# Optimization experiments

Measured on AMD Instinct MI355X. Metric: run time of the kernel, lower is better.

The kernel has to match this reference:

```python
import jax, jax.numpy as jnp
import numpy as np

B, CIN, COUT = 8, 8, 8
NX, NT = 512, 512
M1, M2 = 4, 4


def setup_inputs() -> dict:
    key = jax.random.key(0)
    k1, k2, k3 = jax.random.split(key, 3)
    scale = 1.0 / (CIN * COUT)
    x = jax.random.normal(k1, (B, CIN, NX, NT), dtype=jnp.float32)
    T = jnp.arange(NT, dtype=jnp.float32).reshape(1, NT)  # time grid
    X = jnp.arange(NX, dtype=jnp.float32).reshape(1, NX)  # space grid
    weights1_ri = scale * jax.random.uniform(k2, (CIN, COUT, M1, M2, 2), dtype=jnp.float32)
    weights2_ri = scale * jax.random.uniform(k3, (CIN, COUT, M1, M2, 2), dtype=jnp.float32)
    return {"x": x, "T": T, "X": X, "weights1_ri": weights1_ri, "weights2_ri": weights2_ri}


def reference(x, T, X, weights1_ri, weights2_ri):
    # subsample every other grid point (as in the torch forward)
    xs = x[:, :, ::2, ::2]                      # [B, Cin, Hs, Ws]
    tx = T[:, ::2]                              # [1, Ws]
    ty = X[:, ::2]                              # [1, Hs]
    dty = ty[0, 1] - ty[0, 0]
    dtx = tx[0, 1] - tx[0, 0]
    Hs, Ws = xs.shape[-2], xs.shape[-1]
    Wr = Ws // 2 + 1

    FW1 = jnp.fft.rfft2(xs)                     # [B, Cin, Hs, Wr] complex64

    two_pi_i = 2.0 * jnp.pi * 1j
    lam1 = (jnp.fft.fftfreq(Hs).astype(jnp.float32) / dty).astype(jnp.complex64) * two_pi_i   # [Hs]
    lam2 = (jnp.fft.rfftfreq(Ws).astype(jnp.float32) / dtx).astype(jnp.complex64) * two_pi_i  # [Wr]

    w1 = (weights1_ri[..., 0] + 1j * weights1_ri[..., 1]).astype(jnp.complex64)
    w2 = (weights2_ri[..., 0] + 1j * weights2_ri[..., 1]).astype(jnp.complex64)

    out2 = jnp.zeros((xs.shape[0], w1.shape[1], Hs, Wr), dtype=jnp.complex64)
    out2 = out2.at[:, :, :M1, :M2].set(
        jnp.einsum('bixy,ioxy->boxy', FW1[:, :, :M1, :M2], w1))
    out2 = out2.at[:, :, -M1:, :M2].set(
        jnp.einsum('bixy,ioxy->boxy', FW1[:, :, -M1:, :M2], w2))

    # inverse transform onto the FULL (non-subsampled) grid via complex exponentials.
    # Same math as the original rank-4 term6 einsum, factorized separably.
    E1 = jnp.exp(lam1[:, None] * X.astype(jnp.complex64).reshape(1, -1))  # [Hs, NX]
    E2 = jnp.exp(lam2[:, None] * T.astype(jnp.complex64).reshape(1, -1))  # [Wr, NT]

    tmp = jnp.einsum('boxw,xz->bozw', out2, E1)   # [B, Cout, NX, Wr]
    x2 = jnp.einsum('bozw,wi->bozi', tmp, E2)     # [B, Cout, NX, NT]
    return jnp.real(x2) / (Ws * Hs)
```

## Files before the change

### kernel.cpp

```cpp
#include <hip/hip_runtime.h>
#include <hip/hip_bf16.h>


#define PI2 6.283185307179586f

typedef float vfloat4 __attribute__((ext_vector_type(4)));

__device__ __forceinline__ float foldred(float u, float v, int msk, int lane) {
    float send = (lane & msk) ? u : v;
    float recv = __shfl_xor(send, msk, 64);
    return ((lane & msk) ? v : u) + recv;
}

__device__ __forceinline__ float fold8(const float* ar, const float* ai, int lane) {
    float A0 = foldred(ar[0], ai[0], 1, lane);
    float A1 = foldred(ar[1], ai[1], 1, lane);
    float A2 = foldred(ar[2], ai[2], 1, lane);
    float A3 = foldred(ar[3], ai[3], 1, lane);
    float B0 = foldred(A0, A1, 2, lane);
    float B1 = foldred(A2, A3, 2, lane);
    float C  = foldred(B0, B1, 4, lane);
    C += __shfl_xor(C, 8, 64);
    C += __shfl_xor(C, 16, 64);
    C += __shfl_xor(C, 32, 64);
    return C;
}

__global__ __launch_bounds__(256, 8) void k_fused(const float* __restrict__ x,
                                                  const float* __restrict__ w1,
                                                  const float* __restrict__ w2,
                                                  float* __restrict__ Yg,
                                                  unsigned int* __restrict__ done,
                                                  float* __restrict__ out) {
    __shared__ float vals[4][64];
    __shared__ float lcf[64];

    int lane = threadIdx.x & 63;
    int w    = threadIdx.x >> 6;
    int b    = blockIdx.x & 7;
    int t    = blockIdx.x >> 3;

    {
        int ci = t >> 5, g = t & 31;
        int bc = b * 8 + ci;
        int y0 = g * 8 + w * 2;

        const vfloat4* r0 = (const vfloat4*)(x + ((size_t)bc * 512 + (size_t)(2 * y0)) * 512);
        const vfloat4* r1 = (const vfloat4*)(x + ((size_t)bc * 512 + (size_t)(2 * y0 + 2)) * 512);
        vfloat4 a0 = __builtin_nontemporal_load(&r0[lane]);
        vfloat4 a1 = __builtin_nontemporal_load(&r0[lane + 64]);
        vfloat4 b0 = __builtin_nontemporal_load(&r1[lane]);
        vfloat4 b1 = __builtin_nontemporal_load(&r1[lane + 64]);

        float s, c;
        sincosf((PI2 / 128.0f) * (float)lane, &s, &c);
        float er[4], ei[4], orE[4], oiE[4];
        er[0] = 1.f; ei[0] = 0.f;
        er[1] = c;   ei[1] = -s;
        er[2] = er[1]*er[1] - ei[1]*ei[1];  ei[2] = 2.f*er[1]*ei[1];
        er[3] = er[2]*er[1] - ei[2]*ei[1];  ei[3] = er[2]*ei[1] + ei[2]*er[1];
        const float rr1 = 0.999698818696204f, ri1 = -0.024541228522912f;
        const float rr2 = 0.998795456205172f, ri2 = -0.049067674327418f;
        const float rr3 = 0.997290456678690f, ri3 = -0.073564563599667f;
        orE[0] = 1.f; oiE[0] = 0.f;
        orE[1] = er[1]*rr1 - ei[1]*ri1;  oiE[1] = er[1]*ri1 + ei[1]*rr1;
        orE[2] = er[2]*rr2 - ei[2]*ri2;  oiE[2] = er[2]*ri2 + ei[2]*rr2;
        orE[3] = er[3]*rr3 - ei[3]*ri3;  oiE[3] = er[3]*ri3 + ei[3]*rr3;

        float arA[4], aiA[4], arB[4], aiB[4];
#pragma unroll
        for (int kw = 0; kw < 4; ++kw) {
            float sgn = (kw & 1) ? -1.f : 1.f;
            float eA = a0[0] + sgn * a1[0], oA = a0[2] + sgn * a1[2];
            float eB = b0[0] + sgn * b1[0], oB = b0[2] + sgn * b1[2];
            arA[kw] = eA * er[kw] + oA * orE[kw];
            aiA[kw] = eA * ei[kw] + oA * oiE[kw];
            arB[kw] = eB * er[kw] + oB * orE[kw];
            aiB[kw] = eB * ei[kw] + oB * oiE[kw];
        }
        float Ca = fold8(arA, aiA, lane);
        float Cb = fold8(arB, aiB, lane);

        int midx = lane >> 3;
        float mf = (midx < 4) ? (float)midx : (float)(midx - 8);
        float snm, csm;
        sincosf((PI2 / 256.0f) * mf * (float)y0, &snm, &csm);
        float ty0 = -snm;
        float smm, cmm;
        sincosf((PI2 / 256.0f) * mf, &smm, &cmm);
        float cs1 = csm * cmm + ty0 * smm;
        float ty1 = ty0 * cmm - csm * smm;

        float pa = __shfl_xor(Ca, 1, 64);
        float pb = __shfl_xor(Cb, 1, 64);
        float selA = (lane & 1) ? ty0 : -ty0;
        float selB = (lane & 1) ? ty1 : -ty1;
        vals[w][lane] = Ca * csm + pa * selA + Cb * cs1 + pb * selB;
        __syncthreads();

        if (threadIdx.x < 64) {
            float sum = vals[0][lane] + vals[1][lane] + vals[2][lane] + vals[3][lane];
            __hip_atomic_store(&Yg[((size_t)((b * 32 + g) * 8 + ci)) * 64 + lane], sum,
                               __ATOMIC_RELEASE, __HIP_MEMORY_SCOPE_AGENT);
        }
        __syncthreads();
        if (threadIdx.x == 0)
            __hip_atomic_fetch_add(&done[b], 1u, __ATOMIC_RELEASE, __HIP_MEMORY_SCOPE_AGENT);
    }

    if (threadIdx.x == 0) {
        while (__hip_atomic_load(&done[b], __ATOMIC_ACQUIRE, __HIP_MEMORY_SCOPE_AGENT) < 256u)
            __builtin_amdgcn_s_sleep(2);
    }
    __syncthreads();

    int o     = t >> 5;
    int chunk = t & 31;
    int bo    = b * 8 + o;

    {
        int midx = lane >> 3, kw = (lane >> 1) & 3, ri = lane & 1, mx = midx & 3;
        const float* wt = (midx < 4) ? w1 : w2;
        float wr_[8], swi_[8];
#pragma unroll
        for (int ci = 0; ci < 8; ++ci) {
            const float* wp = wt + ((((ci * 8 + o) * 4 + mx) * 4 + kw) * 2);
            wr_[ci]  = wp[0];
            swi_[ci] = ri ? wp[1] : -wp[1];
        }
        float acc = 0.f;
#pragma unroll
        for (int gi = 0; gi < 8; ++gi) {
            int g = w + gi * 4;
            float* Yp = Yg + ((size_t)((b * 32 + g) * 8)) * 64 + lane;
#pragma unroll
            for (int ci = 0; ci < 8; ++ci) {
                float Yv = __hip_atomic_load(Yp + ci * 64, __ATOMIC_RELAXED,
                                             __HIP_MEMORY_SCOPE_AGENT);
                float pt = __shfl_xor(Yv, 1, 64);
                acc += Yv * wr_[ci] + pt * swi_[ci];
            }
        }
        vals[w][lane] = acc;
    }
    __syncthreads();
    if (w == 0)
        lcf[lane] = vals[0][lane] + vals[1][lane] + vals[2][lane] + vals[3][lane];
    __syncthreads();

    float c1b, s1b;
    sincosf((PI2 / 512.0f) * (float)(lane * 4), &s1b, &c1b);
    const float cr = 0.99992470183839f;
    const float sr = 0.012271538285720f;
    const float inv = 1.0f / 65536.0f;

    int ll = lane & 31;
    int kw = ll & 3, midx = (ll >> 2) & 7;
    float m = (midx < 4) ? (float)midx : (float)(midx - 8);
    float2 cc = make_float2(lcf[(midx * 4 + kw) * 2], lcf[(midx * 4 + kw) * 2 + 1]);
    float sgm = (midx & 1) ? -1.f : 1.f;

#pragma unroll
    for (int e = 0; e < 2; ++e) {
        int z = chunk * 8 + w * 2 + e;

        float ang = (PI2 / 512.0f) * m * (float)z;
        float s, c;
        sincosf(ang, &s, &c);
        float hx = cc.x * c - cc.y * s;
        float hy = cc.x * s + cc.y * c;
        float gx = sgm * hx, gy = sgm * hy;

        float F = foldred(hx, hy, 4, lane);
        F += __shfl_xor(F, 8, 64);
        F += __shfl_xor(F, 16, 64);
        float G = foldred(gx, gy, 4, lane);
        G += __shfl_xor(G, 8, 64);
        G += __shfl_xor(G, 16, 64);
        float h0x = __shfl(F, 0, 64);
        float h1x = __shfl(F, 1, 64), h2x = __shfl(F, 2, 64), h3x = __shfl(F, 3, 64);
        float h1y = __shfl(F, 5, 64), h2y = __shfl(F, 6, 64), h3y = __shfl(F, 7, 64);
        float g0x = __shfl(G, 0, 64);
        float g1x = __shfl(G, 1, 64), g2x = __shfl(G, 2, 64), g3x = __shfl(G, 3, 64);
        float g1y = __shfl(G, 5, 64), g2y = __shfl(G, 6, 64), g3y = __shfl(G, 7, 64);

        float* orow0 = out + (size_t)(bo * 512 + z) * 512;
        float* orow1 = orow0 + 256 * 512;

        float c1 = c1b, s1 = s1b;
        vfloat4 r0, r1, q0, q1;
#pragma unroll
        for (int j = 0; j < 4; ++j) {
            float c2a = c1 * c1 - s1 * s1, s2a = 2.f * c1 * s1;
            float c3a = c2a * c1 - s2a * s1, s3a = s2a * c1 + c2a * s1;
            float t1 = h1x * c1  - h1y * s1;
            float t2 = h2x * c2a - h2y * s2a;
            float t3 = h3x * c3a - h3y * s3a;
            r0[j] = (h0x + t1 + t2 + t3) * inv;
            r1[j] = (h0x - t1 + t2 - t3) * inv;
            float u1 = g1x * c1  - g1y * s1;
            float u2 = g2x * c2a - g2y * s2a;
            float u3 = g3x * c3a - g3y * s3a;
            q0[j] = (g0x + u1 + u2 + u3) * inv;
            q1[j] = (g0x - u1 + u2 - u3) * inv;
            float nc = c1 * cr - s1 * sr;
            float ns = s1 * cr + c1 * sr;
            c1 = nc; s1 = ns;
        }
        __builtin_nontemporal_store(r0, (vfloat4*)(orow0 + lane * 4));
        __builtin_nontemporal_store(r1, (vfloat4*)(orow0 + 256 + lane * 4));
        __builtin_nontemporal_store(q0, (vfloat4*)(orow1 + lane * 4));
        __builtin_nontemporal_store(q1, (vfloat4*)(orow1 + 256 + lane * 4));
    }
}

__global__ __launch_bounds__(256) void k_dft_t(const float* __restrict__ x,
                                               float* __restrict__ Yg) {
    __shared__ float vals[4][64];
    int lane = threadIdx.x & 63;
    int w    = threadIdx.x >> 6;
    int bc   = blockIdx.x >> 4;
    int g    = blockIdx.x & 15;
    int y0   = g * 16 + w * 4;

    const float* base = x + (size_t)bc * 512 * 512;
    vfloat4 A0[4], A1[4];
#pragma unroll
    for (int r = 0; r < 4; ++r) {
        const vfloat4* row = (const vfloat4*)(base + (size_t)(2 * (y0 + r)) * 512);
        A0[r] = __builtin_nontemporal_load(&row[lane]);
        A1[r] = __builtin_nontemporal_load(&row[lane + 64]);
    }
    float s, c;
    sincosf((PI2 / 128.0f) * (float)lane, &s, &c);
    float er[4], ei[4], orE[4], oiE[4];
    er[0] = 1.f; ei[0] = 0.f;
    er[1] = c;   ei[1] = -s;
    er[2] = er[1]*er[1] - ei[1]*ei[1];  ei[2] = 2.f*er[1]*ei[1];
    er[3] = er[2]*er[1] - ei[2]*ei[1];  ei[3] = er[2]*ei[1] + ei[2]*er[1];
    const float rr1 = 0.999698818696204f, ri1 = -0.024541228522912f;
    const float rr2 = 0.998795456205172f, ri2 = -0.049067674327418f;
    const float rr3 = 0.997290456678690f, ri3 = -0.073564563599667f;
    orE[0] = 1.f; oiE[0] = 0.f;
    orE[1] = er[1]*rr1 - ei[1]*ri1;  oiE[1] = er[1]*ri1 + ei[1]*rr1;
    orE[2] = er[2]*rr2 - ei[2]*ri2;  oiE[2] = er[2]*ri2 + ei[2]*rr2;
    orE[3] = er[3]*rr3 - ei[3]*ri3;  oiE[3] = er[3]*ri3 + ei[3]*rr3;

    int midx = lane >> 3;
    float mf = (midx < 4) ? (float)midx : (float)(midx - 8);
    float snm, csm;
    sincosf((PI2 / 256.0f) * mf * (float)y0, &snm, &csm);
    float cs = csm, ty = -snm;
    float smm, cmm;
    sincosf((PI2 / 256.0f) * mf, &smm, &cmm);

    float acc = 0.f;
#pragma unroll
    for (int r = 0; r < 4; ++r) {
        float s0 = A0[r][0] + A1[r][0], d0 = A0[r][0] - A1[r][0];
        float s2 = A0[r][2] + A1[r][2], d2 = A0[r][2] - A1[r][2];
        float ar[4], ai[4];
#pragma unroll
        for (int kw = 0; kw < 4; ++kw) {
            float E = (kw & 1) ? d0 : s0;
            float O = (kw & 1) ? d2 : s2;
            ar[kw] = E * er[kw] + O * orE[kw];
            ai[kw] = E * ei[kw] + O * oiE[kw];
        }
        float C  = fold8(ar, ai, lane);
        float pt = __shfl_xor(C, 1, 64);
        float sel = (lane & 1) ? ty : -ty;
        acc += C * cs + pt * sel;
        float nc = cs * cmm + ty * smm;
        float nt = ty * cmm - cs * smm;
        cs = nc; ty = nt;
    }
    vals[w][lane] = acc;
    __syncthreads();
    if (threadIdx.x < 64) {
        int b = bc >> 3, ci = bc & 7;
        float sum = vals[0][lane] + vals[1][lane] + vals[2][lane] + vals[3][lane];
        Yg[((size_t)((b * 16 + g) * 8 + ci)) * 64 + lane] = sum;
    }
}

__global__ __launch_bounds__(256) void k_mix_eval(const float* __restrict__ Yg,
                                                  const float* __restrict__ w1,
                                                  const float* __restrict__ w2,
                                                  float* __restrict__ out) {
    __shared__ float vals[4][64];
    __shared__ float lcf[64];
    int lane  = threadIdx.x & 63;
    int w     = threadIdx.x >> 6;
    int bo    = blockIdx.x >> 5;
    int chunk = blockIdx.x & 31;
    int b = bo >> 3, o = bo & 7;
    {
        int midx = lane >> 3, kw = (lane >> 1) & 3, ri = lane & 1, mx = midx & 3;
        const float* wt = (midx < 4) ? w1 : w2;
        float wr_[8], swi_[8];
#pragma unroll
        for (int ci = 0; ci < 8; ++ci) {
            const float* wp = wt + ((((ci * 8 + o) * 4 + mx) * 4 + kw) * 2);
            wr_[ci]  = wp[0];
            swi_[ci] = ri ? wp[1] : -wp[1];
        }
        float acc = 0.f;
#pragma unroll
        for (int gi = 0; gi < 4; ++gi) {
            int g = w + gi * 4;
            const float* Yp = Yg + ((size_t)((b * 16 + g) * 8)) * 64 + lane;
#pragma unroll
            for (int ci = 0; ci < 8; ++ci) {
                float Yv = Yp[ci * 64];
                float pt = __shfl_xor(Yv, 1, 64);
                acc += Yv * wr_[ci] + pt * swi_[ci];
            }
        }
        vals[w][lane] = acc;
    }
    __syncthreads();
    if (w == 0)
        lcf[lane] = vals[0][lane] + vals[1][lane] + vals[2][lane] + vals[3][lane];
    __syncthreads();

    float c1b, s1b;
    sincosf((PI2 / 512.0f) * (float)(lane * 4), &s1b, &c1b);
    const float cr = 0.99992470183839f;
    const float sr = 0.012271538285720f;
    const float inv = 1.0f / 65536.0f;
    int ll = lane & 31;
    int kw = ll & 3, midx = (ll >> 2) & 7;
    float m = (midx < 4) ? (float)midx : (float)(midx - 8);
    float2 cc = make_float2(lcf[ll * 2], lcf[ll * 2 + 1]);
    float sgm = (midx & 1) ? -1.f : 1.f;
#pragma unroll
    for (int e = 0; e < 2; ++e) {
        int z = chunk * 8 + w * 2 + e;
        float ang = (PI2 / 512.0f) * m * (float)z;
        float s, c;
        sincosf(ang, &s, &c);
        float hx = cc.x * c - cc.y * s;
        float hy = cc.x * s + cc.y * c;
        float gx = sgm * hx, gy = sgm * hy;
        float F = foldred(hx, hy, 4, lane);
        F += __shfl_xor(F, 8, 64);
        F += __shfl_xor(F, 16, 64);
        float G = foldred(gx, gy, 4, lane);
        G += __shfl_xor(G, 8, 64);
        G += __shfl_xor(G, 16, 64);
        float h0x = __shfl(F, 0, 64);
        float h1x = __shfl(F, 1, 64), h2x = __shfl(F, 2, 64), h3x = __shfl(F, 3, 64);
        float h1y = __shfl(F, 5, 64), h2y = __shfl(F, 6, 64), h3y = __shfl(F, 7, 64);
        float g0x = __shfl(G, 0, 64);
        float g1x = __shfl(G, 1, 64), g2x = __shfl(G, 2, 64), g3x = __shfl(G, 3, 64);
        float g1y = __shfl(G, 5, 64), g2y = __shfl(G, 6, 64), g3y = __shfl(G, 7, 64);
        float* orow0 = out + (size_t)(bo * 512 + z) * 512;
        float* orow1 = orow0 + 256 * 512;
        float c1 = c1b, s1 = s1b;
        vfloat4 r0, r1, q0, q1;
#pragma unroll
        for (int j = 0; j < 4; ++j) {
            float c2a = c1 * c1 - s1 * s1, s2a = 2.f * c1 * s1;
            float c3a = c2a * c1 - s2a * s1, s3a = s2a * c1 + c2a * s1;
            float t1 = h1x * c1  - h1y * s1;
            float t2 = h2x * c2a - h2y * s2a;
            float t3 = h3x * c3a - h3y * s3a;
            r0[j] = (h0x + t1 + t2 + t3) * inv;
            r1[j] = (h0x - t1 + t2 - t3) * inv;
            float u1 = g1x * c1  - g1y * s1;
            float u2 = g2x * c2a - g2y * s2a;
            float u3 = g3x * c3a - g3y * s3a;
            q0[j] = (g0x + u1 + u2 + u3) * inv;
            q1[j] = (g0x - u1 + u2 - u3) * inv;
            float nc = c1 * cr - s1 * sr;
            float ns = s1 * cr + c1 * sr;
            c1 = nc; s1 = ns;
        }
        __builtin_nontemporal_store(r0, (vfloat4*)(orow0 + lane * 4));
        __builtin_nontemporal_store(r1, (vfloat4*)(orow0 + 256 + lane * 4));
        __builtin_nontemporal_store(q0, (vfloat4*)(orow1 + lane * 4));
        __builtin_nontemporal_store(q1, (vfloat4*)(orow1 + 256 + lane * 4));
    }
}

extern "C" void kernel_launch(void* const* d_in, const int* in_sizes, int n_in,
                              void* d_out, int out_size, void* d_ws, size_t ws_size,
                              hipStream_t stream) {
    const float* x  = (const float*)d_in[0];
    const float* w1 = (const float*)d_in[3];
    const float* w2 = (const float*)d_in[4];
    float* out = (float*)d_out;

    float* Yg = (float*)d_ws;
    unsigned int* done = (unsigned int*)(Yg + 131072);

    int maxb = 0;
    bool fused_ok =
        (hipOccupancyMaxActiveBlocksPerMultiprocessor(&maxb, (const void*)k_fused, 256, 0)
             == hipSuccess) && (maxb >= 8);

    if (fused_ok) {
        hipMemsetAsync(done, 0, 8 * sizeof(unsigned int), stream);
        k_fused<<<2048, 256, 0, stream>>>(x, w1, w2, Yg, done, out);
    } else {
        k_dft_t<<<1024, 256, 0, stream>>>(x, Yg);
        k_mix_eval<<<2048, 256, 0, stream>>>(Yg, w1, w2, out);
    }
}
```

Before: 25.71 us.

## Compute channel-mixed coefficients once per (batch,out) and share via flag

Before, all 32 chunk blocks of each (batch, output channel) redundantly read the full Yg slice and did the channel-mixing reduction. Now only chunk 0 computes the 64 mixed coefficients, publishes them to a workspace buffer, and sets a per-(b,o) release flag. The other blocks spin on that flag and load the coefficients. This removes redundant global loads and arithmetic but adds a second inter-block dependency and spin-wait, which can serialise the blocks behind chunk 0.

```diff
diff --git a/kernel.cpp b/kernel.cpp
--- a/kernel.cpp
+++ b/kernel.cpp
@@ -30,7 +30,9 @@
                                                   const float* __restrict__ w1,
                                                   const float* __restrict__ w2,
                                                   float* __restrict__ Yg,
+                                                  float* __restrict__ c2f,
                                                   unsigned int* __restrict__ done,
+                                                  unsigned int* __restrict__ flag2,
                                                   float* __restrict__ out) {
     __shared__ float vals[4][64];
     __shared__ float lcf[64];
@@ -118,7 +120,7 @@
     int chunk = t & 31;
     int bo    = b * 8 + o;
 
-    {
+    if (chunk == 0) {
         int midx = lane >> 3, kw = (lane >> 1) & 3, ri = lane & 1, mx = midx & 3;
         const float* wt = (midx < 4) ? w1 : w2;
         float wr_[8], swi_[8];
@@ -142,11 +144,27 @@
             }
         }
         vals[w][lane] = acc;
-    }
-    __syncthreads();
-    if (w == 0)
-        lcf[lane] = vals[0][lane] + vals[1][lane] + vals[2][lane] + vals[3][lane];
-    __syncthreads();
+        __syncthreads();
+        if (w == 0) {
+            float v = vals[0][lane] + vals[1][lane] + vals[2][lane] + vals[3][lane];
+            lcf[lane] = v;
+            __hip_atomic_store(&c2f[bo * 64 + lane], v,
+                               __ATOMIC_RELEASE, __HIP_MEMORY_SCOPE_AGENT);
+        }
+        __syncthreads();
+        if (threadIdx.x == 0)
+            __hip_atomic_store(&flag2[bo], 1u, __ATOMIC_RELEASE, __HIP_MEMORY_SCOPE_AGENT);
+    } else {
+        if (threadIdx.x == 0) {
+            while (__hip_atomic_load(&flag2[bo], __ATOMIC_ACQUIRE, __HIP_MEMORY_SCOPE_AGENT) < 1u)
+                __builtin_amdgcn_s_sleep(2);
+        }
+        __syncthreads();
+        if (threadIdx.x < 64)
+            lcf[threadIdx.x] = __hip_atomic_load(&c2f[bo * 64 + threadIdx.x],
+                                                 __ATOMIC_RELAXED, __HIP_MEMORY_SCOPE_AGENT);
+        __syncthreads();
+    }
 
     float c1b, s1b;
     sincosf((PI2 / 512.0f) * (float)(lane * 4), &s1b, &c1b);
@@ -392,8 +410,10 @@
     const float* w2 = (const float*)d_in[4];
     float* out = (float*)d_out;
 
-    float* Yg = (float*)d_ws;
-    unsigned int* done = (unsigned int*)(Yg + 131072);
+    float* Yg  = (float*)d_ws;
+    float* c2f = Yg + 131072;
+    unsigned int* done  = (unsigned int*)(c2f + 4096);
+    unsigned int* flag2 = done + 8;
 
     int maxb = 0;
     bool fused_ok =
@@ -401,8 +421,8 @@
              == hipSuccess) && (maxb >= 8);
 
     if (fused_ok) {
-        hipMemsetAsync(done, 0, 8 * sizeof(unsigned int), stream);
-        k_fused<<<2048, 256, 0, stream>>>(x, w1, w2, Yg, done, out);
+        hipMemsetAsync(done, 0, 72 * sizeof(unsigned int), stream);
+        k_fused<<<2048, 256, 0, stream>>>(x, w1, w2, Yg, c2f, done, flag2, out);
     } else {
         k_dft_t<<<1024, 256, 0, stream>>>(x, Yg);
         k_mix_eval<<<2048, 256, 0, stream>>>(Yg, w1, w2, out);
```

Result: no change. 25.62 us (-0.4%).

## Split fused kernel into producer and consumer blocks with per-batch flags

Applied to the files above, without the earlier changes.

Replaces the all-blocks-do-both fused kernel with a pipelined kernel. The first 512 blocks each run two forward-DFT tasks and signal a per-batch counter. The remaining 1536 blocks wait only on their own batch's counter, then mix weights and evaluate the output, so output writes for early batches can overlap with DFT work on later ones. It also swaps sincosf for hardware sin/cos on revolution-normalised arguments, which is cheaper but slightly less accurate. This relies on producer blocks being resident and scheduled before consumers spin, guarded by the occupancy check.

```diff
diff --git a/kernel.cpp b/kernel.cpp
--- a/kernel.cpp
+++ b/kernel.cpp
@@ -5,6 +5,12 @@
 #define PI2 6.283185307179586f
 
 typedef float vfloat4 __attribute__((ext_vector_type(4)));
+
+__device__ __forceinline__ void fsincos(float r, float* s, float* c) {
+    r = r - floorf(r);
+    *s = __builtin_amdgcn_sinf(r);
+    *c = __builtin_amdgcn_cosf(r);
+}
 
 __device__ __forceinline__ float foldred(float u, float v, int msk, int lane) {
     float send = (lane & msk) ? u : v;
@@ -26,202 +32,13 @@
     return C;
 }
 
-__global__ __launch_bounds__(256, 8) void k_fused(const float* __restrict__ x,
-                                                  const float* __restrict__ w1,
-                                                  const float* __restrict__ w2,
-                                                  float* __restrict__ Yg,
-                                                  unsigned int* __restrict__ done,
-                                                  float* __restrict__ out) {
-    __shared__ float vals[4][64];
-    __shared__ float lcf[64];
-
-    int lane = threadIdx.x & 63;
-    int w    = threadIdx.x >> 6;
-    int b    = blockIdx.x & 7;
-    int t    = blockIdx.x >> 3;
-
-    {
-        int ci = t >> 5, g = t & 31;
-        int bc = b * 8 + ci;
-        int y0 = g * 8 + w * 2;
-
-        const vfloat4* r0 = (const vfloat4*)(x + ((size_t)bc * 512 + (size_t)(2 * y0)) * 512);
-        const vfloat4* r1 = (const vfloat4*)(x + ((size_t)bc * 512 + (size_t)(2 * y0 + 2)) * 512);
-        vfloat4 a0 = __builtin_nontemporal_load(&r0[lane]);
-        vfloat4 a1 = __builtin_nontemporal_load(&r0[lane + 64]);
-        vfloat4 b0 = __builtin_nontemporal_load(&r1[lane]);
-        vfloat4 b1 = __builtin_nontemporal_load(&r1[lane + 64]);
-
-        float s, c;
-        sincosf((PI2 / 128.0f) * (float)lane, &s, &c);
-        float er[4], ei[4], orE[4], oiE[4];
-        er[0] = 1.f; ei[0] = 0.f;
-        er[1] = c;   ei[1] = -s;
-        er[2] = er[1]*er[1] - ei[1]*ei[1];  ei[2] = 2.f*er[1]*ei[1];
-        er[3] = er[2]*er[1] - ei[2]*ei[1];  ei[3] = er[2]*ei[1] + ei[2]*er[1];
-        const float rr1 = 0.999698818696204f, ri1 = -0.024541228522912f;
-        const float rr2 = 0.998795456205172f, ri2 = -0.049067674327418f;
-        const float rr3 = 0.997290456678690f, ri3 = -0.073564563599667f;
-        orE[0] = 1.f; oiE[0] = 0.f;
-        orE[1] = er[1]*rr1 - ei[1]*ri1;  oiE[1] = er[1]*ri1 + ei[1]*rr1;
-        orE[2] = er[2]*rr2 - ei[2]*ri2;  oiE[2] = er[2]*ri2 + ei[2]*rr2;
-        orE[3] = er[3]*rr3 - ei[3]*ri3;  oiE[3] = er[3]*ri3 + ei[3]*rr3;
-
-        float arA[4], aiA[4], arB[4], aiB[4];
-#pragma unroll
-        for (int kw = 0; kw < 4; ++kw) {
-            float sgn = (kw & 1) ? -1.f : 1.f;
-            float eA = a0[0] + sgn * a1[0], oA = a0[2] + sgn * a1[2];
-            float eB = b0[0] + sgn * b1[0], oB = b0[2] + sgn * b1[2];
-            arA[kw] = eA * er[kw] + oA * orE[kw];
-            aiA[kw] = eA * ei[kw] + oA * oiE[kw];
-            arB[kw] = eB * er[kw] + oB * orE[kw];
-            aiB[kw] = eB * ei[kw] + oB * oiE[kw];
-        }
-        float Ca = fold8(arA, aiA, lane);
-        float Cb = fold8(arB, aiB, lane);
-
-        int midx = lane >> 3;
-        float mf = (midx < 4) ? (float)midx : (float)(midx - 8);
-        float snm, csm;
-        sincosf((PI2 / 256.0f) * mf * (float)y0, &snm, &csm);
-        float ty0 = -snm;
-        float smm, cmm;
-        sincosf((PI2 / 256.0f) * mf, &smm, &cmm);
-        float cs1 = csm * cmm + ty0 * smm;
-        float ty1 = ty0 * cmm - csm * smm;
-
-        float pa = __shfl_xor(Ca, 1, 64);
-        float pb = __shfl_xor(Cb, 1, 64);
-        float selA = (lane & 1) ? ty0 : -ty0;
-        float selB = (lane & 1) ? ty1 : -ty1;
-        vals[w][lane] = Ca * csm + pa * selA + Cb * cs1 + pb * selB;
-        __syncthreads();
-
-        if (threadIdx.x < 64) {
-            float sum = vals[0][lane] + vals[1][lane] + vals[2][lane] + vals[3][lane];
-            __hip_atomic_store(&Yg[((size_t)((b * 32 + g) * 8 + ci)) * 64 + lane], sum,
-                               __ATOMIC_RELEASE, __HIP_MEMORY_SCOPE_AGENT);
-        }
-        __syncthreads();
-        if (threadIdx.x == 0)
-            __hip_atomic_fetch_add(&done[b], 1u, __ATOMIC_RELEASE, __HIP_MEMORY_SCOPE_AGENT);
-    }
-
-    if (threadIdx.x == 0) {
-        while (__hip_atomic_load(&done[b], __ATOMIC_ACQUIRE, __HIP_MEMORY_SCOPE_AGENT) < 256u)
-            __builtin_amdgcn_s_sleep(2);
-    }
-    __syncthreads();
-
-    int o     = t >> 5;
-    int chunk = t & 31;
-    int bo    = b * 8 + o;
-
-    {
-        int midx = lane >> 3, kw = (lane >> 1) & 3, ri = lane & 1, mx = midx & 3;
-        const float* wt = (midx < 4) ? w1 : w2;
-        float wr_[8], swi_[8];
-#pragma unroll
-        for (int ci = 0; ci < 8; ++ci) {
-            const float* wp = wt + ((((ci * 8 + o) * 4 + mx) * 4 + kw) * 2);
-            wr_[ci]  = wp[0];
-            swi_[ci] = ri ? wp[1] : -wp[1];
-        }
-        float acc = 0.f;
-#pragma unroll
-        for (int gi = 0; gi < 8; ++gi) {
-            int g = w + gi * 4;
-            float* Yp = Yg + ((size_t)((b * 32 + g) * 8)) * 64 + lane;
-#pragma unroll
-            for (int ci = 0; ci < 8; ++ci) {
-                float Yv = __hip_atomic_load(Yp + ci * 64, __ATOMIC_RELAXED,
-                                             __HIP_MEMORY_SCOPE_AGENT);
-                float pt = __shfl_xor(Yv, 1, 64);
-                acc += Yv * wr_[ci] + pt * swi_[ci];
-            }
-        }
-        vals[w][lane] = acc;
-    }
-    __syncthreads();
-    if (w == 0)
-        lcf[lane] = vals[0][lane] + vals[1][lane] + vals[2][lane] + vals[3][lane];
-    __syncthreads();
-
-    float c1b, s1b;
-    sincosf((PI2 / 512.0f) * (float)(lane * 4), &s1b, &c1b);
-    const float cr = 0.99992470183839f;
-    const float sr = 0.012271538285720f;
-    const float inv = 1.0f / 65536.0f;
-
-    int ll = lane & 31;
-    int kw = ll & 3, midx = (ll >> 2) & 7;
-    float m = (midx < 4) ? (float)midx : (float)(midx - 8);
-    float2 cc = make_float2(lcf[(midx * 4 + kw) * 2], lcf[(midx * 4 + kw) * 2 + 1]);
-    float sgm = (midx & 1) ? -1.f : 1.f;
-
-#pragma unroll
-    for (int e = 0; e < 2; ++e) {
-        int z = chunk * 8 + w * 2 + e;
-
-        float ang = (PI2 / 512.0f) * m * (float)z;
-        float s, c;
-        sincosf(ang, &s, &c);
-        float hx = cc.x * c - cc.y * s;
-        float hy = cc.x * s + cc.y * c;
-        float gx = sgm * hx, gy = sgm * hy;
-
-        float F = foldred(hx, hy, 4, lane);
-        F += __shfl_xor(F, 8, 64);
-        F += __shfl_xor(F, 16, 64);
-        float G = foldred(gx, gy, 4, lane);
-        G += __shfl_xor(G, 8, 64);
-        G += __shfl_xor(G, 16, 64);
-        float h0x = __shfl(F, 0, 64);
-        float h1x = __shfl(F, 1, 64), h2x = __shfl(F, 2, 64), h3x = __shfl(F, 3, 64);
-        float h1y = __shfl(F, 5, 64), h2y = __shfl(F, 6, 64), h3y = __shfl(F, 7, 64);
-        float g0x = __shfl(G, 0, 64);
-        float g1x = __shfl(G, 1, 64), g2x = __shfl(G, 2, 64), g3x = __shfl(G, 3, 64);
-        float g1y = __shfl(G, 5, 64), g2y = __shfl(G, 6, 64), g3y = __shfl(G, 7, 64);
-
-        float* orow0 = out + (size_t)(bo * 512 + z) * 512;
-        float* orow1 = orow0 + 256 * 512;
-
-        float c1 = c1b, s1 = s1b;
-        vfloat4 r0, r1, q0, q1;
-#pragma unroll
-        for (int j = 0; j < 4; ++j) {
-            float c2a = c1 * c1 - s1 * s1, s2a = 2.f * c1 * s1;
-            float c3a = c2a * c1 - s2a * s1, s3a = s2a * c1 + c2a * s1;
-            float t1 = h1x * c1  - h1y * s1;
-            float t2 = h2x * c2a - h2y * s2a;
-            float t3 = h3x * c3a - h3y * s3a;
-            r0[j] = (h0x + t1 + t2 + t3) * inv;
-            r1[j] = (h0x - t1 + t2 - t3) * inv;
-            float u1 = g1x * c1  - g1y * s1;
-            float u2 = g2x * c2a - g2y * s2a;
-            float u3 = g3x * c3a - g3y * s3a;
-            q0[j] = (g0x + u1 + u2 + u3) * inv;
-            q1[j] = (g0x - u1 + u2 - u3) * inv;
-            float nc = c1 * cr - s1 * sr;
-            float ns = s1 * cr + c1 * sr;
-            c1 = nc; s1 = ns;
-        }
-        __builtin_nontemporal_store(r0, (vfloat4*)(orow0 + lane * 4));
-        __builtin_nontemporal_store(r1, (vfloat4*)(orow0 + 256 + lane * 4));
-        __builtin_nontemporal_store(q0, (vfloat4*)(orow1 + lane * 4));
-        __builtin_nontemporal_store(q1, (vfloat4*)(orow1 + 256 + lane * 4));
-    }
-}
-
-__global__ __launch_bounds__(256) void k_dft_t(const float* __restrict__ x,
-                                               float* __restrict__ Yg) {
-    __shared__ float vals[4][64];
-    int lane = threadIdx.x & 63;
-    int w    = threadIdx.x >> 6;
-    int bc   = blockIdx.x >> 4;
-    int g    = blockIdx.x & 15;
-    int y0   = g * 16 + w * 4;
+__device__ __forceinline__ void dft_task(const float* __restrict__ x,
+                                         float* __restrict__ Yg,
+                                         float vals[4][64],
+                                         int task, int lane, int w) {
+    int bc = task >> 4;
+    int g  = task & 15;
+    int y0 = g * 16 + w * 4;
 
     const float* base = x + (size_t)bc * 512 * 512;
     vfloat4 A0[4], A1[4];
@@ -231,8 +48,9 @@
         A0[r] = __builtin_nontemporal_load(&row[lane]);
         A1[r] = __builtin_nontemporal_load(&row[lane + 64]);
     }
+
     float s, c;
-    sincosf((PI2 / 128.0f) * (float)lane, &s, &c);
+    fsincos((float)lane * 0.0078125f, &s, &c);
     float er[4], ei[4], orE[4], oiE[4];
     er[0] = 1.f; ei[0] = 0.f;
     er[1] = c;   ei[1] = -s;
@@ -249,10 +67,222 @@
     int midx = lane >> 3;
     float mf = (midx < 4) ? (float)midx : (float)(midx - 8);
     float snm, csm;
-    sincosf((PI2 / 256.0f) * mf * (float)y0, &snm, &csm);
+    fsincos(mf * (float)y0 * 0.00390625f, &snm, &csm);
     float cs = csm, ty = -snm;
     float smm, cmm;
-    sincosf((PI2 / 256.0f) * mf, &smm, &cmm);
+    fsincos(mf * 0.00390625f, &smm, &cmm);
+
+    float acc = 0.f;
+#pragma unroll
+    for (int r = 0; r < 4; ++r) {
+        float s0 = A0[r][0] + A1[r][0], d0 = A0[r][0] - A1[r][0];
+        float s2 = A0[r][2] + A1[r][2], d2 = A0[r][2] - A1[r][2];
+        float ar[4], ai[4];
+#pragma unroll
+        for (int kw = 0; kw < 4; ++kw) {
+            float E = (kw & 1) ? d0 : s0;
+            float O = (kw & 1) ? d2 : s2;
+            ar[kw] = E * er[kw] + O * orE[kw];
+            ai[kw] = E * ei[kw] + O * oiE[kw];
+        }
+        float C  = fold8(ar, ai, lane);
+        float pt = __shfl_xor(C, 1, 64);
+        float sel = (lane & 1) ? ty : -ty;
+        acc += C * cs + pt * sel;
+        float nc = cs * cmm + ty * smm;
+        float nt = ty * cmm - cs * smm;
+        cs = nc; ty = nt;
+    }
+    vals[w][lane] = acc;
+    __syncthreads();
+
+    if (w == 0) {
+        int b = bc >> 3, ci = bc & 7;
+        float sum = vals[0][lane] + vals[1][lane] + vals[2][lane] + vals[3][lane];
+        __hip_atomic_store(&Yg[((size_t)((b * 16 + g) * 8 + ci)) * 64 + lane], sum,
+                           __ATOMIC_RELEASE, __HIP_MEMORY_SCOPE_AGENT);
+    }
+    __syncthreads();
+}
+
+__global__ __launch_bounds__(256, 8) void k_pipe(const float* __restrict__ x,
+                                                 const float* __restrict__ w1,
+                                                 const float* __restrict__ w2,
+                                                 float* __restrict__ Yg,
+                                                 unsigned int* __restrict__ done,
+                                                 float* __restrict__ out) {
+    __shared__ float vals[4][64];
+    __shared__ float lcf[64];
+
+    int lane = threadIdx.x & 63;
+    int w    = threadIdx.x >> 6;
+    int blk  = blockIdx.x;
+
+    if (blk < 512) {
+#pragma unroll
+        for (int rnd = 0; rnd < 2; ++rnd) {
+            int task = blk + rnd * 512;
+            dft_task(x, Yg, vals, task, lane, w);
+            if (threadIdx.x == 0) {
+                int b = task >> 7;
+                __hip_atomic_fetch_add(&done[b], 1u, __ATOMIC_RELEASE,
+                                       __HIP_MEMORY_SCOPE_AGENT);
+            }
+        }
+        return;
+    }
+
+    int cb = blk - 512;
+    int ntask = (cb < 512) ? 2 : 1;
+
+    float c1b, s1b;
+    fsincos((float)lane * 0.0078125f, &s1b, &c1b);
+    const float cr = 0.99992470183839f;
+    const float sr = 0.012271538285720f;
+    const float inv = 1.0f / 65536.0f;
+
+    for (int q = 0; q < ntask; ++q) {
+        int e = cb + q * 1536;
+        int bo = e >> 5, chunk = e & 31;
+        int b = bo >> 3, o = bo & 7;
+
+        if (threadIdx.x == 0) {
+            while (__hip_atomic_load(&done[b], __ATOMIC_ACQUIRE,
+                                     __HIP_MEMORY_SCOPE_AGENT) < 128u)
+                __builtin_amdgcn_s_sleep(2);
+        }
+        __syncthreads();
+
+        {
+            int midx = lane >> 3, kw = (lane >> 1) & 3, ri = lane & 1, mx = midx & 3;
+            const float* wt = (midx < 4) ? w1 : w2;
+            float wr_[8], swi_[8];
+#pragma unroll
+            for (int ci = 0; ci < 8; ++ci) {
+                const float* wp = wt + ((((ci * 8 + o) * 4 + mx) * 4 + kw) * 2);
+                wr_[ci]  = wp[0];
+                swi_[ci] = ri ? wp[1] : -wp[1];
+            }
+            float acc = 0.f;
+#pragma unroll
+            for (int gi = 0; gi < 4; ++gi) {
+                int g = w + gi * 4;
+                float* Yp = Yg + ((size_t)((b * 16 + g) * 8)) * 64 + lane;
+#pragma unroll
+                for (int ci = 0; ci < 8; ++ci) {
+                    float Yv = __hip_atomic_load(Yp + ci * 64, __ATOMIC_RELAXED,
+                                                 __HIP_MEMORY_SCOPE_AGENT);
+                    float pt = __shfl_xor(Yv, 1, 64);
+                    acc += Yv * wr_[ci] + pt * swi_[ci];
+                }
+            }
+            vals[w][lane] = acc;
+        }
+        __syncthreads();
+        if (w == 0)
+            lcf[lane] = vals[0][lane] + vals[1][lane] + vals[2][lane] + vals[3][lane];
+        __syncthreads();
+
+        int ll = lane & 31;
+        int kw = ll & 3, midx = (ll >> 2) & 7;
+        float m = (midx < 4) ? (float)midx : (float)(midx - 8);
+        float2 cc = make_float2(lcf[(midx * 4 + kw) * 2], lcf[(midx * 4 + kw) * 2 + 1]);
+        float sgm = (midx & 1) ? -1.f : 1.f;
+
+#pragma unroll
+        for (int ez = 0; ez < 2; ++ez) {
+            int z = chunk * 8 + w * 2 + ez;
+
+            float s, c;
+            fsincos(m * (float)z * 0.001953125f, &s, &c);
+            float hx = cc.x * c - cc.y * s;
+            float hy = cc.x * s + cc.y * c;
+            float gx = sgm * hx, gy = sgm * hy;
+
+            float F = foldred(hx, hy, 4, lane);
+            F += __shfl_xor(F, 8, 64);
+            F += __shfl_xor(F, 16, 64);
+            float G = foldred(gx, gy, 4, lane);
+            G += __shfl_xor(G, 8, 64);
+            G += __shfl_xor(G, 16, 64);
+            float h0x = __shfl(F, 0, 64);
+            float h1x = __shfl(F, 1, 64), h2x = __shfl(F, 2, 64), h3x = __shfl(F, 3, 64);
+            float h1y = __shfl(F, 5, 64), h2y = __shfl(F, 6, 64), h3y = __shfl(F, 7, 64);
+            float g0x = __shfl(G, 0, 64);
+            float g1x = __shfl(G, 1, 64), g2x = __shfl(G, 2, 64), g3x = __shfl(G, 3, 64);
+            float g1y = __shfl(G, 5, 64), g2y = __shfl(G, 6, 64), g3y = __shfl(G, 7, 64);
+
+            float* orow0 = out + (size_t)(bo * 512 + z) * 512;
+            float* orow1 = orow0 + 256 * 512;
+
+            float c1 = c1b, s1 = s1b;
+            vfloat4 r0, r1, q0, q1;
+#pragma unroll
+            for (int j = 0; j < 4; ++j) {
+                float c2a = c1 * c1 - s1 * s1, s2a = 2.f * c1 * s1;
+                float c3a = c2a * c1 - s2a * s1, s3a = s2a * c1 + c2a * s1;
+                float t1 = h1x * c1  - h1y * s1;
+                float t2 = h2x * c2a - h2y * s2a;
+                float t3 = h3x * c3a - h3y * s3a;
+                r0[j] = (h0x + t1 + t2 + t3) * inv;
+                r1[j] = (h0x - t1 + t2 - t3) * inv;
+                float u1 = g1x * c1  - g1y * s1;
+                float u2 = g2x * c2a - g2y * s2a;
+                float u3 = g3x * c3a - g3y * s3a;
+                q0[j] = (g0x + u1 + u2 + u3) * inv;
+                q1[j] = (g0x - u1 + u2 - u3) * inv;
+                float nc = c1 * cr - s1 * sr;
+                float ns = s1 * cr + c1 * sr;
+                c1 = nc; s1 = ns;
+            }
+            __builtin_nontemporal_store(r0, (vfloat4*)(orow0 + lane * 4));
+            __builtin_nontemporal_store(r1, (vfloat4*)(orow0 + 256 + lane * 4));
+            __builtin_nontemporal_store(q0, (vfloat4*)(orow1 + lane * 4));
+            __builtin_nontemporal_store(q1, (vfloat4*)(orow1 + 256 + lane * 4));
+        }
+        __syncthreads();
+    }
+}
+
+__global__ __launch_bounds__(256) void k_dft_t(const float* __restrict__ x,
+                                               float* __restrict__ Yg) {
+    __shared__ float vals[4][64];
+    int lane = threadIdx.x & 63;
+    int w    = threadIdx.x >> 6;
+    int task = blockIdx.x;
+    int bc = task >> 4, g = task & 15;
+    int y0 = g * 16 + w * 4;
+
+    const float* base = x + (size_t)bc * 512 * 512;
+    vfloat4 A0[4], A1[4];
+#pragma unroll
+    for (int r = 0; r < 4; ++r) {
+        const vfloat4* row = (const vfloat4*)(base + (size_t)(2 * (y0 + r)) * 512);
+        A0[r] = __builtin_nontemporal_load(&row[lane]);
+        A1[r] = __builtin_nontemporal_load(&row[lane + 64]);
+    }
+    float s, c;
+    fsincos((float)lane * 0.0078125f, &s, &c);
+    float er[4], ei[4], orE[4], oiE[4];
+    er[0] = 1.f; ei[0] = 0.f;
+    er[1] = c;   ei[1] = -s;
+    er[2] = er[1]*er[1] - ei[1]*ei[1];  ei[2] = 2.f*er[1]*ei[1];
+    er[3] = er[2]*er[1] - ei[2]*ei[1];  ei[3] = er[2]*ei[1] + ei[2]*er[1];
+    const float rr1 = 0.999698818696204f, ri1 = -0.024541228522912f;
+    const float rr2 = 0.998795456205172f, ri2 = -0.049067674327418f;
+    const float rr3 = 0.997290456678690f, ri3 = -0.073564563599667f;
+    orE[0] = 1.f; oiE[0] = 0.f;
+    orE[1] = er[1]*rr1 - ei[1]*ri1;  oiE[1] = er[1]*ri1 + ei[1]*rr1;
+    orE[2] = er[2]*rr2 - ei[2]*ri2;  oiE[2] = er[2]*ri2 + ei[2]*rr2;
+    orE[3] = er[3]*rr3 - ei[3]*ri3;  oiE[3] = er[3]*ri3 + ei[3]*rr3;
+
+    int midx = lane >> 3;
+    float mf = (midx < 4) ? (float)midx : (float)(midx - 8);
+    float snm, csm;
+    fsincos(mf * (float)y0 * 0.00390625f, &snm, &csm);
+    float cs = csm, ty = -snm;
+    float smm, cmm;
+    fsincos(mf * 0.00390625f, &smm, &cmm);
 
     float acc = 0.f;
 #pragma unroll
@@ -325,7 +355,7 @@
     __syncthreads();
 
     float c1b, s1b;
-    sincosf((PI2 / 512.0f) * (float)(lane * 4), &s1b, &c1b);
+    fsincos((float)lane * 0.0078125f, &s1b, &c1b);
     const float cr = 0.99992470183839f;
     const float sr = 0.012271538285720f;
     const float inv = 1.0f / 65536.0f;
@@ -337,9 +367,8 @@
 #pragma unroll
     for (int e = 0; e < 2; ++e) {
         int z = chunk * 8 + w * 2 + e;
-        float ang = (PI2 / 512.0f) * m * (float)z;
         float s, c;
-        sincosf(ang, &s, &c);
+        fsincos(m * (float)z * 0.001953125f, &s, &c);
         float hx = cc.x * c - cc.y * s;
         float hy = cc.x * s + cc.y * c;
         float gx = sgm * hx, gy = sgm * hy;
@@ -393,16 +422,16 @@
     float* out = (float*)d_out;
 
     float* Yg = (float*)d_ws;
-    unsigned int* done = (unsigned int*)(Yg + 131072);
+    unsigned int* done = (unsigned int*)(Yg + 65536);
 
     int maxb = 0;
-    bool fused_ok =
-        (hipOccupancyMaxActiveBlocksPerMultiprocessor(&maxb, (const void*)k_fused, 256, 0)
+    bool pipe_ok =
+        (hipOccupancyMaxActiveBlocksPerMultiprocessor(&maxb, (const void*)k_pipe, 256, 0)
              == hipSuccess) && (maxb >= 8);
 
-    if (fused_ok) {
+    if (pipe_ok) {
         hipMemsetAsync(done, 0, 8 * sizeof(unsigned int), stream);
-        k_fused<<<2048, 256, 0, stream>>>(x, w1, w2, Yg, done, out);
+        k_pipe<<<2048, 256, 0, stream>>>(x, w1, w2, Yg, done, out);
     } else {
         k_dft_t<<<1024, 256, 0, stream>>>(x, Yg);
         k_mix_eval<<<2048, 256, 0, stream>>>(Yg, w1, w2, out);
```

New measurement: 24.54 us. 1.05x faster.
